# Optimization experiments

Measured on AMD Instinct MI355X. Metric: run time of the kernel, lower is better.

Reference implementation:

```python
import jax, jax.numpy as jnp
import numpy as np
from jax import lax

ROWS, COLS, HID = 5, 5, 4
N = ROWS * COLS
NUM_NEURONS = 128


def _nbr_indices(i, direction):
    # Faithful to get_neighbor_hidden, including the row-wrap behavior of
    # 'col-1'/'col+1' (no column bounds check in the original code).
    row, col = divmod(i, COLS)
    up = (row - 1) * COLS + col
    dn = (row + 1) * COLS + col
    lf = row * COLS + col - 1
    rt = row * COLS + col + 1
    return [up, dn, lf, rt] if direction == 'f' else [up, dn, rt, lf]


def _gather_neighbors(h, idxs):
    # h: (N, bs, HID); returns (bs, 4) of the 4th hidden feature per neighbor
    bs = h.shape[1]
    cols_list = [h[j][:, 3] if 0 <= j < N else jnp.zeros((bs,), h.dtype) for j in idxs]
    return jnp.stack(cols_list, axis=1)


def _make_step(Wx, Wh, Wn, b, direction):
    # One timestep: nodes updated sequentially (node i sees already-updated
    # up/left neighbors within the same timestep, matching the torch loop).
    def step(carry, x_t):  # x_t: (N, bs)
        h, c = carry  # each (N, bs, HID)
        for i in range(N):
            nb = _gather_neighbors(h, _nbr_indices(i, direction))  # (bs,4)
            gates = x_t[i][:, None] @ Wx + h[i] @ Wh + nb @ Wn + b  # (bs,4H)
            ig, fg, og, cc = jnp.split(gates, 4, axis=1)
            nc = jax.nn.sigmoid(fg) * c[i] + jax.nn.sigmoid(ig) * jnp.tanh(cc)
            nh = jax.nn.sigmoid(og) * jnp.tanh(nc)
            h = h.at[i].set(nh)
            c = c.at[i].set(nc)
        return (h, c), None
    return step


def _forward(x, h0f, c0f, h0b, c0b, Wx_f, Wh_f, Wn_f, b_f,
             Wx_b, Wh_b, Wn_b, b_b, W_ff, b_ff, W_out, b_out):
    bs = x.shape[0]
    x_seq = jnp.transpose(x, (2, 1, 0))  # (T, N, bs)
    (hf, cf), _ = lax.scan(_make_step(Wx_f, Wh_f, Wn_f, b_f, 'f'), (h0f, c0f), x_seq)
    (hb, cb), _ = lax.scan(_make_step(Wx_b, Wh_b, Wn_b, b_b, 'b'), (h0b, c0b), x_seq[::-1])
    H_fwd = jnp.transpose(hf, (1, 0, 2))  # (bs, N, HID)
    H_bwd = jnp.transpose(hb, (1, 0, 2))
    H = jnp.concatenate([H_fwd, H_bwd], axis=2).reshape(bs, -1)  # (bs, 200)
    ff = jax.nn.sigmoid(H @ W_ff + b_ff)
    return jax.nn.softmax(ff @ W_out + b_out, axis=1)


def setup_inputs() -> dict:
    key = jax.random.key(0)
    ks = jax.random.split(key, 16)
    bs, T = 8192, 128
    d = {}
    d['x'] = jax.random.normal(ks[0], (bs, N, T), jnp.float32)
    for nm, k in zip(['h0f', 'c0f', 'h0b', 'c0b'], ks[1:5]):
        d[nm] = jax.random.normal(k, (N, bs, HID), jnp.float32) * 0.01
    def lin(k, i, o):
        return jax.random.normal(k, (i, o), jnp.float32) * (1.0 / np.sqrt(i))
    d['Wx_f'] = lin(ks[5], 1, 4 * HID)
    d['Wh_f'] = lin(ks[6], HID, 4 * HID)
    d['Wn_f'] = lin(ks[7], 4, 4 * HID)
    d['b_f'] = jnp.zeros((4 * HID,), jnp.float32)
    d['Wx_b'] = lin(ks[8], 1, 4 * HID)
    d['Wh_b'] = lin(ks[9], HID, 4 * HID)
    d['Wn_b'] = lin(ks[10], 4, 4 * HID)
    d['b_b'] = jnp.zeros((4 * HID,), jnp.float32)
    d['W_ff'] = lin(ks[11], N * 2 * HID, NUM_NEURONS)
    d['b_ff'] = jnp.zeros((NUM_NEURONS,), jnp.float32)
    d['W_out'] = lin(ks[12], NUM_NEURONS, 2)
    d['b_out'] = jnp.zeros((2,), jnp.float32)
    return d


def reference(x, h0f, c0f, h0b, c0b, Wx_f, Wh_f, Wn_f, b_f,
              Wx_b, Wh_b, Wn_b, b_b, W_ff, b_ff, W_out, b_out):
    return _forward(x, h0f, c0f, h0b, c0b, Wx_f, Wh_f, Wn_f, b_f,
                    Wx_b, Wh_b, Wn_b, b_b, W_ff, b_ff, W_out, b_out)
```

## Files before the change

kernel.cpp:

```cpp
#include <hip/hip_runtime.h>
#include <stddef.h>

#define BS 8192
#define NNODE 25
#define TT 128
#define LOG2E 1.4426950408889634f

typedef float v2f __attribute__((ext_vector_type(2)));

__device__ __forceinline__ float ex2(float x) { return __builtin_amdgcn_exp2f(x); }
__device__ __forceinline__ float rcp_(float x) { return __builtin_amdgcn_rcpf(x); }

__device__ float g_hf[NNODE * BS * 4];
__device__ float g_hb[NNODE * BS * 4];

template <int K>
__device__ __forceinline__ float bcast4(float v) {
  int s = __builtin_bit_cast(int, v);
  int r = __builtin_amdgcn_update_dpp(0, s, (K * 0x55), 0xF, 0xF, true);
  return __builtin_bit_cast(float, r);
}

__device__ __forceinline__ void acc2(v2f& A, v2f& B, float s, v2f wa, v2f wb) {
  v2f sv = {s, s};
  A = __builtin_elementwise_fma(sv, wa, A);
  B = __builtin_elementwise_fma(sv, wb, B);
}

template <int DIR>
__device__ __forceinline__ void rnn_run(
    int d, int b, const float* __restrict__ x,
    const float* __restrict__ h0, const float* __restrict__ c0,
    const float* __restrict__ Wx, const float* __restrict__ Wh,
    const float* __restrict__ Wn, const float* __restrict__ Bb,
    float* __restrict__ ho) {
  const int cI = d, cF = 4 + d, cO = 8 + d, cC = 12 + d;
  const float sS = -LOG2E, sC = 2.0f * LOG2E;

  v2f wA[9], wB[9];
  wA[0] = v2f{sS * Wx[cI], sS * Wx[cF]};
  wB[0] = v2f{sS * Wx[cO], sC * Wx[cC]};
#pragma unroll
  for (int k = 0; k < 4; ++k) {
    wA[1 + k] = v2f{sS * Wh[k * 16 + cI], sS * Wh[k * 16 + cF]};
    wB[1 + k] = v2f{sS * Wh[k * 16 + cO], sC * Wh[k * 16 + cC]};
  }
  const int nrow[4] = {0, 1, DIR ? 3 : 2, DIR ? 2 : 3};
#pragma unroll
  for (int k = 0; k < 4; ++k) {
    wA[5 + k] = v2f{sS * Wn[nrow[k] * 16 + cI], sS * Wn[nrow[k] * 16 + cF]};
    wB[5 + k] = v2f{sS * Wn[nrow[k] * 16 + cO], sC * Wn[nrow[k] * 16 + cC]};
  }
  const v2f bA = {sS * Bb[cI], sS * Bb[cF]};
  const v2f bB = {sS * Bb[cO], sC * Bb[cC]};

  float h[NNODE], c[NNODE], b3[NNODE];
#pragma unroll
  for (int i = 0; i < NNODE; ++i) {
    h[i] = h0[(i * BS + b) * 4 + d];
    c[i] = c0[(i * BS + b) * 4 + d];
    b3[i] = bcast4<3>(h[i]);
  }

  const float* xrow = x + (size_t)b * (NNODE * TT);

  for (int blk = 0; blk < TT / 2; ++blk) {
    const int tbase = DIR ? (TT - 2 - 2 * blk) : (2 * blk);
    v2f xv[NNODE];
#pragma unroll
    for (int i = 0; i < NNODE; ++i)
      xv[i] = *(const v2f*)(xrow + i * TT + tbase);

#pragma unroll
    for (int k = 0; k < 2; ++k) {
#pragma unroll
      for (int i = 0; i < NNODE; ++i) {
        const float xval =
            (((DIR ? (1 - k) : k) == 0) ? xv[i].x : xv[i].y);
        const float f0 = bcast4<0>(h[i]);
        const float f1 = bcast4<1>(h[i]);
        const float f2 = bcast4<2>(h[i]);

        v2f A = bA, B = bB;
        acc2(A, B, xval, wA[0], wB[0]);
        acc2(A, B, f0, wA[1], wB[1]);
        acc2(A, B, f1, wA[2], wB[2]);
        acc2(A, B, f2, wA[3], wB[3]);
        acc2(A, B, b3[i], wA[4], wB[4]);
        if (i >= 5) acc2(A, B, b3[i - 5], wA[5], wB[5]);
        if (i < 20) acc2(A, B, b3[i + 5], wA[6], wB[6]);
        if (i >= 1) acc2(A, B, b3[i - 1], wA[7], wB[7]);
        if (i < 24) acc2(A, B, b3[i + 1], wA[8], wB[8]);

        const float Ei = ex2(A.x);
        const float Ef = ex2(A.y);
        const float Eo = ex2(B.x);
        const float Ec = ex2(B.y);
        const float Di = 1.0f + Ei;
        const float Df = 1.0f + Ef;
        const float P = Di * (Ec + 1.0f);
        const float num = fmaf(c[i], P, (Ec - 1.0f) * Df);
        const float nc = num * rcp_(Df * P);
        const float En = ex2(-2.0f * LOG2E * nc);
        const float hn = (1.0f - En) * rcp_((1.0f + En) * (1.0f + Eo));
        c[i] = nc;
        h[i] = hn;
        b3[i] = bcast4<3>(hn);
      }
    }
  }

#pragma unroll
  for (int i = 0; i < NNODE; ++i) ho[(i * BS + b) * 4 + d] = h[i];
}

__global__ __launch_bounds__(256, 1) void rnn_kernel(
    const float* __restrict__ x,
    const float* __restrict__ h0f, const float* __restrict__ c0f,
    const float* __restrict__ h0b, const float* __restrict__ c0b,
    const float* __restrict__ Wxf, const float* __restrict__ Whf,
    const float* __restrict__ Wnf, const float* __restrict__ bf,
    const float* __restrict__ Wxb, const float* __restrict__ Whb,
    const float* __restrict__ Wnb, const float* __restrict__ bb_) {
  const int d = threadIdx.x & 3;
  const int b = blockIdx.x * 64 + (threadIdx.x >> 2);
  if (blockIdx.y == 0) {
    rnn_run<0>(d, b, x, h0f, c0f, Wxf, Whf, Wnf, bf, g_hf);
  } else {
    rnn_run<1>(d, b, x, h0b, c0b, Wxb, Whb, Wnb, bb_, g_hb);
  }
}

__global__ __launch_bounds__(128) void ff_kernel(
    const float* __restrict__ Wff, const float* __restrict__ bff,
    const float* __restrict__ Wout, const float* __restrict__ bout,
    float* __restrict__ out) {
  __shared__ float Hs[8][200];
  __shared__ float ffs[8][129];
  const int tid = threadIdx.x;
  const int b0 = blockIdx.x * 8;

  for (int idx = tid; idx < 8 * 200; idx += 128) {
    const int bb = idx / 200;
    const int k = idx - bb * 200;
    const int i = k >> 3;
    const int dd = k & 7;
    const int b = b0 + bb;
    Hs[bb][k] = (dd < 4) ? g_hf[(i * BS + b) * 4 + dd]
                         : g_hb[(i * BS + b) * 4 + (dd - 4)];
  }
  __syncthreads();

  float acc[8];
  const float bv = bff[tid];
#pragma unroll
  for (int bb = 0; bb < 8; ++bb) acc[bb] = bv;
  for (int k = 0; k < 200; ++k) {
    const float w = Wff[k * 128 + tid];
#pragma unroll
    for (int bb = 0; bb < 8; ++bb) acc[bb] = fmaf(Hs[bb][k], w, acc[bb]);
  }
#pragma unroll
  for (int bb = 0; bb < 8; ++bb)
    ffs[bb][tid] = rcp_(1.0f + ex2(-LOG2E * acc[bb]));
  __syncthreads();

  if (tid < 8) {
    float z0 = bout[0], z1 = bout[1];
    for (int n = 0; n < 128; ++n) {
      const float f = ffs[tid][n];
      z0 = fmaf(f, Wout[n * 2 + 0], z0);
      z1 = fmaf(f, Wout[n * 2 + 1], z1);
    }
    const float m = fmaxf(z0, z1);
    const float e0 = ex2(LOG2E * (z0 - m)), e1 = ex2(LOG2E * (z1 - m));
    const float s = rcp_(e0 + e1);
    out[(size_t)(b0 + tid) * 2 + 0] = e0 * s;
    out[(size_t)(b0 + tid) * 2 + 1] = e1 * s;
  }
}

extern "C" void kernel_launch(void* const* d_in, const int* in_sizes, int n_in,
                              void* d_out, int out_size, void* d_ws, size_t ws_size,
                              hipStream_t stream) {
  (void)in_sizes; (void)n_in; (void)out_size; (void)d_ws; (void)ws_size;
  const float* x    = (const float*)d_in[0];
  const float* h0f  = (const float*)d_in[1];
  const float* c0f  = (const float*)d_in[2];
  const float* h0b  = (const float*)d_in[3];
  const float* c0b  = (const float*)d_in[4];
  const float* Wxf  = (const float*)d_in[5];
  const float* Whf  = (const float*)d_in[6];
  const float* Wnf  = (const float*)d_in[7];
  const float* bf   = (const float*)d_in[8];
  const float* Wxb  = (const float*)d_in[9];
  const float* Whb  = (const float*)d_in[10];
  const float* Wnb  = (const float*)d_in[11];
  const float* bb   = (const float*)d_in[12];
  const float* Wff  = (const float*)d_in[13];
  const float* bff  = (const float*)d_in[14];
  const float* Wout = (const float*)d_in[15];
  const float* bout = (const float*)d_in[16];
  float* out = (float*)d_out;

  rnn_kernel<<<dim3(128, 2), dim3(256), 0, stream>>>(
      x, h0f, c0f, h0b, c0b, Wxf, Whf, Wnf, bf, Wxb, Whb, Wnb, bb);
  ff_kernel<<<dim3(1024), dim3(128), 0, stream>>>(Wff, bff, Wout, bout, out);
}
```

Baseline: 643.0 us.

## Stage input time chunks through shared memory with coalesced vector loads

Instead of each thread reading strided v2f pairs of x straight from global memory every two timesteps, the block now cooperatively loads 16-timestep chunks for its 64 batch rows with coalesced float4 loads. It transposes them into a padded LDS buffer and then reads per-timestep values from LDS. This is meant to cut uncoalesced global traffic and duplicate reads across the 4 lanes that share a batch row. It adds two barriers per chunk and about 104KB of LDS, and the timestep loop is no longer unrolled.

Result: faster. 580.5 us (-9.7%).

```diff
diff --git a/kernel.cpp b/kernel.cpp
--- a/kernel.cpp
+++ b/kernel.cpp
@@ -4,9 +4,13 @@
 #define BS 8192
 #define NNODE 25
 #define TT 128
+#define TCH 16
+#define NW (TT / TCH)
+#define XPAD 65
 #define LOG2E 1.4426950408889634f
 
 typedef float v2f __attribute__((ext_vector_type(2)));
+typedef float v4f __attribute__((ext_vector_type(4)));
 
 __device__ __forceinline__ float ex2(float x) { return __builtin_amdgcn_exp2f(x); }
 __device__ __forceinline__ float rcp_(float x) { return __builtin_amdgcn_rcpf(x); }
@@ -29,11 +33,13 @@
 
 template <int DIR>
 __device__ __forceinline__ void rnn_run(
-    int d, int b, const float* __restrict__ x,
+    int tid, const float* __restrict__ xblk, float* __restrict__ xs,
     const float* __restrict__ h0, const float* __restrict__ c0,
     const float* __restrict__ Wx, const float* __restrict__ Wh,
     const float* __restrict__ Wn, const float* __restrict__ Bb,
-    float* __restrict__ ho) {
+    float* __restrict__ ho, int b) {
+  const int d = tid & 3;
+  const int bl = tid >> 2;
   const int cI = d, cF = 4 + d, cO = 8 + d, cC = 12 + d;
   const float sS = -LOG2E, sC = 2.0f * LOG2E;
 
@@ -62,27 +68,40 @@
     b3[i] = bcast4<3>(h[i]);
   }
 
-  const float* xrow = x + (size_t)b * (NNODE * TT);
-
-  for (int blk = 0; blk < TT / 2; ++blk) {
-    const int tbase = DIR ? (TT - 2 - 2 * blk) : (2 * blk);
-    v2f xv[NNODE];
-#pragma unroll
-    for (int i = 0; i < NNODE; ++i)
-      xv[i] = *(const v2f*)(xrow + i * TT + tbase);
-
-#pragma unroll
-    for (int k = 0; k < 2; ++k) {
+  const int t4 = tid & 3;
+  const int s0 = tid >> 2;
+
+  for (int w = 0; w < NW; ++w) {
+    __syncthreads();
+#pragma unroll
+    for (int r = 0; r < NNODE; ++r) {
+      const int seg = s0 + 64 * r;
+      const int sbl = seg / 25;
+      const int sii = seg - sbl * 25;
+      const int tb = (DIR ? (TT - TCH - TCH * w) : (TCH * w)) + 4 * t4;
+      const v4f v = *(const v4f*)(xblk + ((size_t)sbl * NNODE + sii) * TT + tb);
+#pragma unroll
+      for (int j = 0; j < 4; ++j) {
+        const int kk = DIR ? (15 - 4 * t4 - j) : (4 * t4 + j);
+        xs[(kk * NNODE + sii) * XPAD + sbl] = v[j];
+      }
+    }
+    __syncthreads();
+
+#pragma unroll 1
+    for (int kk = 0; kk < TCH; ++kk) {
+      float xq[NNODE];
+#pragma unroll
+      for (int i = 0; i < NNODE; ++i) xq[i] = xs[(kk * NNODE + i) * XPAD + bl];
+
 #pragma unroll
       for (int i = 0; i < NNODE; ++i) {
-        const float xval =
-            (((DIR ? (1 - k) : k) == 0) ? xv[i].x : xv[i].y);
         const float f0 = bcast4<0>(h[i]);
         const float f1 = bcast4<1>(h[i]);
         const float f2 = bcast4<2>(h[i]);
 
         v2f A = bA, B = bB;
-        acc2(A, B, xval, wA[0], wB[0]);
+        acc2(A, B, xq[i], wA[0], wB[0]);
         acc2(A, B, f0, wA[1], wB[1]);
         acc2(A, B, f1, wA[2], wB[2]);
         acc2(A, B, f2, wA[3], wB[3]);
@@ -122,12 +141,14 @@
     const float* __restrict__ Wnf, const float* __restrict__ bf,
     const float* __restrict__ Wxb, const float* __restrict__ Whb,
     const float* __restrict__ Wnb, const float* __restrict__ bb_) {
-  const int d = threadIdx.x & 3;
-  const int b = blockIdx.x * 64 + (threadIdx.x >> 2);
+  __shared__ float xs[TCH * NNODE * XPAD];
+  const int tid = threadIdx.x;
+  const int b = blockIdx.x * 64 + (tid >> 2);
+  const float* xblk = x + (size_t)(blockIdx.x * 64) * (NNODE * TT);
   if (blockIdx.y == 0) {
-    rnn_run<0>(d, b, x, h0f, c0f, Wxf, Whf, Wnf, bf, g_hf);
+    rnn_run<0>(tid, xblk, xs, h0f, c0f, Wxf, Whf, Wnf, bf, g_hf, b);
   } else {
-    rnn_run<1>(d, b, x, h0b, c0b, Wxb, Whb, Wnb, bb_, g_hb);
+    rnn_run<1>(tid, xblk, xs, h0b, c0b, Wxb, Whb, Wnb, bb_, g_hb, b);
   }
 }
 
```
